# Kernel optimization log

Measured on AMD Instinct MI355X. Metric: run time of the kernel, lower is better.

The kernel has to match this reference:

```python
import jax, jax.numpy as jnp
import numpy as np

NUM_HEADS = 16
EPS = 1e-6

def _rmsnorm(h, w):
    h32 = h.astype(jnp.float32)
    var = jnp.mean(h32 * h32, axis=-1, keepdims=True)
    return (w * (h32 * jax.lax.rsqrt(var + EPS))).astype(h.dtype)

def setup_inputs() -> dict:
    key = jax.random.key(0)
    ks = jax.random.split(key, 4)
    B, N, C = 16, 1024, 1024
    x = jax.random.normal(ks[0], (B, N, C), dtype=jnp.float32)
    qkv_w = jax.random.normal(ks[1], (3 * C, C), dtype=jnp.float32) * (C ** -0.5)
    proj_w = jax.random.normal(ks[2], (C, C), dtype=jnp.float32) * (C ** -0.5)
    proj_b = jnp.zeros((C,), dtype=jnp.float32)
    q_norm_w = jnp.ones((C // NUM_HEADS,), dtype=jnp.float32)
    k_norm_w = jnp.ones((C // NUM_HEADS,), dtype=jnp.float32)
    return {"x": x, "qkv_w": qkv_w, "proj_w": proj_w, "proj_b": proj_b,
            "q_norm_w": q_norm_w, "k_norm_w": k_norm_w}

def reference(x, qkv_w, proj_w, proj_b, q_norm_w, k_norm_w):
    B, N, C = x.shape
    H = NUM_HEADS
    Dh = C // H
    scale = Dh ** -0.5  # qk_scale default; temperature = 1.0
    # QKV projection (no bias): [B,N,3,H,Dh]
    qkv = (x @ qkv_w.T).reshape(B, N, 3, H, Dh)
    q, k, v = qkv[:, :, 0], qkv[:, :, 1], qkv[:, :, 2]
    # per-head QK RMSNorm (fp32 internally)
    q = _rmsnorm(q, q_norm_w)
    k = _rmsnorm(k, k_norm_w)
    # explicit softmax attention: [B,H,N,N]
    attn = jnp.einsum('bnhd,bmhd->bhnm', q * scale, k)
    attn = jax.nn.softmax(attn, axis=-1)
    out = jnp.einsum('bhnm,bmhd->bnhd', attn, v).reshape(B, N, C)
    return out @ proj_w.T + proj_b
```

## Files before the change

kernel.cpp:

```cpp
#include <hip/hip_runtime.h>
#include <hip/hip_bf16.h>

typedef __attribute__((ext_vector_type(8))) __bf16 bf16x8;
typedef __attribute__((ext_vector_type(4))) __bf16 bf16x4;
typedef __attribute__((ext_vector_type(4))) float f32x4;

#define AS1(p) ((__attribute__((address_space(1))) void*)(p))
#define AS3(p) ((__attribute__((address_space(3))) void*)(p))

__global__ void f2b_kernel(const float4* __restrict__ in, bf16x4* __restrict__ out, int n4) {
    int idx = blockIdx.x * blockDim.x + threadIdx.x;
    int stride = gridDim.x * blockDim.x;
    for (int i = idx; i < n4; i += stride) {
        float4 v = in[i];
        bf16x4 o;
        o[0] = (__bf16)v.x; o[1] = (__bf16)v.y; o[2] = (__bf16)v.z; o[3] = (__bf16)v.w;
        out[i] = o;
    }
}

template<int MODE>
__global__ __launch_bounds__(512, 2)
void gemm256(const __bf16* __restrict__ A, const __bf16* __restrict__ Bw,
             const float* __restrict__ bias, const float* __restrict__ qw,
             const float* __restrict__ kw, float* __restrict__ Cf,
             __bf16* __restrict__ Cb, __bf16* __restrict__ Vt,
             int M, int K, int nbn, int ldc)
{
    __shared__ __bf16 Asl[4][256 * 32];
    __shared__ __bf16 Bsl[4][256 * 32];
    const int tid = threadIdx.x, l = tid & 63, w = tid >> 6;
    const int fr = l & 15, fk = l >> 4;

    const int cpx = gridDim.x >> 3;
    const int wg = (blockIdx.x & 7) * cpx + (blockIdx.x >> 3);
    const int bm = wg / nbn, bn = wg % nbn;

    const __bf16* Ag = A + (size_t)bm * 256 * K;
    const __bf16* Bg = Bw + (size_t)bn * 256 * K;

    const int arow = tid >> 2;
    const int uch = (tid & 3) ^ (arow & 3) ^ ((arow >> 2) & 3);
    const size_t ga = (size_t)arow * K + uch * 8;
    const size_t ga2 = ga + (size_t)128 * K;

    const int axc = (fk ^ (fr & 3) ^ ((fr >> 2) & 3)) * 16;
    int aoff[8], boff[4];
    #pragma unroll
    for (int m = 0; m < 8; ++m)
        aoff[m] = ((w >> 2) * 128 + m * 16 + fr) * 64 + axc;
    #pragma unroll
    for (int n = 0; n < 4; ++n)
        boff[n] = ((w & 3) * 64 + n * 16 + fr) * 64 + axc;

    f32x4 acc[8][4] = {};

#define STAGE256(S) do {                                                                    \
    const int sb_ = (S) & 3;                                                                \
    __builtin_amdgcn_global_load_lds(AS1(Ag + (size_t)(S) * 32 + ga),                       \
        AS3((char*)&Asl[sb_][0] + tid * 16), 16, 0, 0);                                     \
    __builtin_amdgcn_global_load_lds(AS1(Ag + (size_t)(S) * 32 + ga2),                      \
        AS3((char*)&Asl[sb_][0] + tid * 16 + 8192), 16, 0, 0);                              \
    __builtin_amdgcn_global_load_lds(AS1(Bg + (size_t)(S) * 32 + ga),                       \
        AS3((char*)&Bsl[sb_][0] + tid * 16), 16, 0, 0);                                     \
    __builtin_amdgcn_global_load_lds(AS1(Bg + (size_t)(S) * 32 + ga2),                      \
        AS3((char*)&Bsl[sb_][0] + tid * 16 + 8192), 16, 0, 0);                              \
} while (0)

#define PHASE256(S, VMSTR, DOSTAGE) do {                                                    \
    asm volatile("s_waitcnt vmcnt(" VMSTR ")" ::: "memory");                                \
    __builtin_amdgcn_s_barrier();                                                           \
    __builtin_amdgcn_sched_barrier(0);                                                      \
    const int pb_ = (S) & 3;                                                                \
    bf16x8 af[8], bfv[4];                                                                   \
    _Pragma("unroll")                                                                       \
    for (int m = 0; m < 8; ++m)                                                             \
        af[m] = *(const bf16x8*)((const char*)&Asl[pb_][0] + aoff[m]);                      \
    _Pragma("unroll")                                                                       \
    for (int n = 0; n < 4; ++n)                                                             \
        bfv[n] = *(const bf16x8*)((const char*)&Bsl[pb_][0] + boff[n]);                     \
    if (DOSTAGE) STAGE256((S) + 3);                                                         \
    __builtin_amdgcn_s_setprio(1);                                                          \
    _Pragma("unroll")                                                                       \
    for (int m = 0; m < 8; ++m)                                                             \
        _Pragma("unroll")                                                                   \
        for (int n = 0; n < 4; ++n)                                                         \
            acc[m][n] = __builtin_amdgcn_mfma_f32_16x16x32_bf16(af[m], bfv[n], acc[m][n], 0, 0, 0); \
    __builtin_amdgcn_s_setprio(0);                                                          \
} while (0)

    const int S = K >> 5;
    STAGE256(0); STAGE256(1); STAGE256(2);
    for (int s = 0; s < S - 2; ++s)
        PHASE256(s, "8", (s + 3 < S));
    PHASE256(S - 2, "4", false);
    PHASE256(S - 1, "0", false);
#undef PHASE256
#undef STAGE256

    const int rb0 = bm * 256 + (w >> 2) * 128 + fk * 4;
    const int cb0 = bn * 256 + (w & 3) * 64;

    if (MODE == 1) {
        #pragma unroll
        for (int m = 0; m < 8; ++m)
            #pragma unroll
            for (int n = 0; n < 4; ++n) {
                const int col = cb0 + n * 16 + fr;
                const float bv = bias[col];
                #pragma unroll
                for (int r = 0; r < 4; ++r)
                    Cf[(size_t)(rb0 + m * 16 + r) * ldc + col] = acc[m][n][r] + bv;
            }
    } else {
        const int sect = bn >> 2;
        if (sect < 2) {
            const float* wp = (sect == 0) ? qw : kw;
            float wn[4];
            #pragma unroll
            for (int n = 0; n < 4; ++n) wn[n] = wp[((w & 3) * 64 + n * 16 + fr) & 63];
            #pragma unroll
            for (int m = 0; m < 8; ++m) {
                float sc[4];
                #pragma unroll
                for (int r = 0; r < 4; ++r) {
                    float ps = 0.f;
                    #pragma unroll
                    for (int n = 0; n < 4; ++n) ps += acc[m][n][r] * acc[m][n][r];
                    ps += __shfl_xor(ps, 1); ps += __shfl_xor(ps, 2);
                    ps += __shfl_xor(ps, 4); ps += __shfl_xor(ps, 8);
                    sc[r] = rsqrtf(ps * (1.0f / 64.0f) + 1e-6f);
                    if (sect == 0) sc[r] *= 0.18033688011112042f;
                }
                #pragma unroll
                for (int n = 0; n < 4; ++n)
                    #pragma unroll
                    for (int r = 0; r < 4; ++r)
                        Cb[(size_t)(rb0 + m * 16 + r) * ldc + cb0 + n * 16 + fr] =
                            (__bf16)(acc[m][n][r] * sc[r] * wn[n]);
            }
        } else {
            #pragma unroll
            for (int m = 0; m < 8; ++m) {
                const int tok = rb0 + m * 16;
                const int b = tok >> 10, ntok = tok & 1023;
                #pragma unroll
                for (int n = 0; n < 4; ++n) {
                    const int vd = (bn - 8) * 256 + (w & 3) * 64 + n * 16 + fr;
                    bf16x4 pk;
                    #pragma unroll
                    for (int r = 0; r < 4; ++r) pk[r] = (__bf16)acc[m][n][r];
                    *(bf16x4*)&Vt[((size_t)((b * 16 + (vd >> 6)) * 64 + (vd & 63))) * 1024 + ntok] = pk;
                }
            }
        }
    }
}

__global__ __launch_bounds__(256, 3)
void attn_kernel(const __bf16* __restrict__ qkv, const __bf16* __restrict__ vt,
                 __bf16* __restrict__ ao)
{
    __shared__ __bf16 Ks[2][64 * 64];
    __shared__ __bf16 Vs[2][64 * 64];
    __shared__ __bf16 Pl[4][16 * 64];
    const int tid = threadIdx.x, l = tid & 63, w = tid >> 6;
    const int fr = l & 15, fk = l >> 4;
    const int sw = (fr & 7) << 4;

    const int bi = blockIdx.x;
    const int L = (bi & 7) * 256 + (bi >> 3);
    const int qb = L & 7, h = (L >> 3) & 15, b = L >> 7;

    const __bf16* Kg = qkv + (size_t)b * 1024 * 2048 + 1024 + h * 64;
    const __bf16* Vg = vt + (size_t)((b * 16 + h) * 64) * 1024;
    const int srow = tid >> 3, scp = tid & 7;

    const int c8 = (scp ^ (srow & 7)) * 8;
    const size_t kO0 = (size_t)srow * 2048 + c8, kO1 = kO0 + 32 * 2048;
    const size_t vO0 = (size_t)srow * 1024 + c8, vO1 = vO0 + 32 * 1024;
    char* ksd = (char*)&Ks[0][0] + tid * 16;
    char* vsd = (char*)&Vs[0][0] + tid * 16;

#define STAGE(KP, VP, BUF) do {                                                           \
    __builtin_amdgcn_global_load_lds(AS1((KP) + kO0), AS3(ksd + (BUF) * 8192), 16, 0, 0); \
    __builtin_amdgcn_global_load_lds(AS1((KP) + kO1), AS3(ksd + (BUF) * 8192 + 4096), 16, 0, 0); \
    __builtin_amdgcn_global_load_lds(AS1((VP) + vO0), AS3(vsd + (BUF) * 8192), 16, 0, 0); \
    __builtin_amdgcn_global_load_lds(AS1((VP) + vO1), AS3(vsd + (BUF) * 8192 + 4096), 16, 0, 0); \
} while (0)

    STAGE(Kg, Vg, 0);

    const int qrow0 = b * 1024 + qb * 128 + w * 32;
    bf16x8 qf[2][2];
    #pragma unroll
    for (int qi = 0; qi < 2; ++qi)
        #pragma unroll
        for (int dc = 0; dc < 2; ++dc)
            qf[qi][dc] = *(const bf16x8*)&qkv[(size_t)(qrow0 + qi * 16 + fr) * 2048
                                              + h * 64 + dc * 32 + fk * 8];

    const int kb0 = fr * 128 + ((fk ^ (fr & 7)) * 16);
    const int kb1 = fr * 128 + (((4 + fk) ^ (fr & 7)) * 16);
    const char* KsB = (const char*)&Ks[0][0];
    const char* VsB = (const char*)&Vs[0][0];

    char* Pw = (char*)&Pl[w][0];
    const int pw0 = (fr * 128 + 0 * 32 + fk * 8) ^ sw;
    const int pw1 = (fr * 128 + 1 * 32 + fk * 8) ^ sw;
    const int pw2 = (fr * 128 + 2 * 32 + fk * 8) ^ sw;
    const int pw3 = (fr * 128 + 3 * 32 + fk * 8) ^ sw;
    const int pr0 = (fr * 128 + 0 * 64 + fk * 16) ^ sw;
    const int pr1 = (fr * 128 + 1 * 64 + fk * 16) ^ sw;

    bf16x8 onesf;
    #pragma unroll
    for (int i = 0; i < 8; ++i) onesf[i] = (__bf16)1.0f;

    f32x4 oacc[2][4] = {};
    f32x4 lacc[2] = {};

    const __bf16* kg = Kg;
    const __bf16* vg = Vg;
    __syncthreads();

    for (int kt = 0; kt < 16; ++kt) {
        const int cur = kt & 1;
        if (kt < 15) { kg += 64 * 2048; vg += 64; STAGE(kg, vg, cur ^ 1); }

        const int cb = cur * 8192;
        bf16x8 kf[4][2], vf[4][2];
        #pragma unroll
        for (int n = 0; n < 4; ++n) {
            kf[n][0] = *(const bf16x8*)(KsB + cb + kb0 + n * 2048);
            kf[n][1] = *(const bf16x8*)(KsB + cb + kb1 + n * 2048);
        }
        #pragma unroll
        for (int nd = 0; nd < 4; ++nd) {
            vf[nd][0] = *(const bf16x8*)(VsB + cb + kb0 + nd * 2048);
            vf[nd][1] = *(const bf16x8*)(VsB + cb + kb1 + nd * 2048);
        }

        #pragma unroll
        for (int qi = 0; qi < 2; ++qi) {
            f32x4 sacc[4] = {};
            #pragma unroll
            for (int n = 0; n < 4; ++n)
                #pragma unroll
                for (int dc = 0; dc < 2; ++dc)
                    sacc[n] = __builtin_amdgcn_mfma_f32_16x16x32_bf16(kf[n][dc], qf[qi][dc],
                                                                      sacc[n], 0, 0, 0);

            #pragma unroll
            for (int n = 0; n < 4; ++n) {
                bf16x4 pk;
                #pragma unroll
                for (int r = 0; r < 4; ++r)
                    pk[r] = (__bf16)__builtin_amdgcn_exp2f(sacc[n][r]);
                const int pwn = (n == 0) ? pw0 : (n == 1) ? pw1 : (n == 2) ? pw2 : pw3;
                *(bf16x4*)(Pw + pwn) = pk;
            }

            bf16x8 pf0 = *(const bf16x8*)(Pw + pr0);
            bf16x8 pf1 = *(const bf16x8*)(Pw + pr1);
            lacc[qi] = __builtin_amdgcn_mfma_f32_16x16x32_bf16(pf0, onesf, lacc[qi], 0, 0, 0);
            lacc[qi] = __builtin_amdgcn_mfma_f32_16x16x32_bf16(pf1, onesf, lacc[qi], 0, 0, 0);
            #pragma unroll
            for (int nd = 0; nd < 4; ++nd) {
                oacc[qi][nd] = __builtin_amdgcn_mfma_f32_16x16x32_bf16(pf0, vf[nd][0],
                                                                       oacc[qi][nd], 0, 0, 0);
                oacc[qi][nd] = __builtin_amdgcn_mfma_f32_16x16x32_bf16(pf1, vf[nd][1],
                                                                       oacc[qi][nd], 0, 0, 0);
            }
        }
        __syncthreads();
    }

    #pragma unroll
    for (int qi = 0; qi < 2; ++qi) {
        float inv[4];
        #pragma unroll
        for (int r = 0; r < 4; ++r)
            inv[r] = __builtin_amdgcn_rcpf(lacc[qi][r]);
        #pragma unroll
        for (int nd = 0; nd < 4; ++nd)
            #pragma unroll
            for (int r = 0; r < 4; ++r)
                ao[(size_t)(qrow0 + qi * 16 + fk * 4 + r) * 1024 + h * 64 + nd * 16 + fr] =
                    (__bf16)(oacc[qi][nd][r] * inv[r]);
    }
#undef STAGE
}

extern "C" void kernel_launch(void* const* d_in, const int* in_sizes, int n_in,
                              void* d_out, int out_size, void* d_ws, size_t ws_size,
                              hipStream_t stream)
{
    const float* x      = (const float*)d_in[0];
    const float* qkv_w  = (const float*)d_in[1];
    const float* proj_w = (const float*)d_in[2];
    const float* proj_b = (const float*)d_in[3];
    const float* qnw    = (const float*)d_in[4];
    const float* knw    = (const float*)d_in[5];

    char* ws = (char*)d_ws;
    __bf16* xb    = (__bf16*)(ws);
    __bf16* wqkv  = (__bf16*)(ws + 33554432);
    __bf16* wproj = (__bf16*)(ws + 39845888);
    __bf16* qkv   = (__bf16*)(ws + 41943040);
    __bf16* vt    = (__bf16*)(ws + 109051904);
    __bf16* ao    = (__bf16*)(ws + 142606336);

    f2b_kernel<<<2048, 256, 0, stream>>>((const float4*)x,      (bf16x4*)xb,    16777216 / 4);
    f2b_kernel<<<2048, 256, 0, stream>>>((const float4*)qkv_w,  (bf16x4*)wqkv,  3145728 / 4);
    f2b_kernel<<<1024, 256, 0, stream>>>((const float4*)proj_w, (bf16x4*)wproj, 1048576 / 4);

    gemm256<0><<<768, 512, 0, stream>>>(xb, wqkv, nullptr, qnw, knw,
                                        nullptr, qkv, vt, 16384, 1024, 12, 2048);
    attn_kernel<<<2048, 256, 0, stream>>>(qkv, vt, ao);
    gemm256<1><<<256, 512, 0, stream>>>(ao, wproj, proj_b, nullptr, nullptr,
                                        (float*)d_out, nullptr, nullptr, 16384, 1024, 4, 1024);
}
```

Measured before the change: 264.8 us.

## Restructure gemm256 main loop into interleaved half-tile load/MFMA pipeline

Replaces the 4-stage K=32 ring buffer with double-buffered K=64 tiles split into two halves. Global-to-LDS loads for the next halves are interleaved between four MFMA quads per iteration, and fragment registers are halved to 4 A and 4 B vectors. The LDS swizzle pattern changes and launch bounds drop to one block per SM. The aim is better overlap of memory and MFMA work with lower register pressure, at the cost of extra barriers and possibly lower occupancy.

After: 269.5 us. About the same (+1.8%).

```diff
diff --git a/kernel.cpp b/kernel.cpp
--- a/kernel.cpp
+++ b/kernel.cpp
@@ -20,15 +20,15 @@
 }
 
 template<int MODE>
-__global__ __launch_bounds__(512, 2)
+__global__ __launch_bounds__(512, 1)
 void gemm256(const __bf16* __restrict__ A, const __bf16* __restrict__ Bw,
              const float* __restrict__ bias, const float* __restrict__ qw,
              const float* __restrict__ kw, float* __restrict__ Cf,
              __bf16* __restrict__ Cb, __bf16* __restrict__ Vt,
              int M, int K, int nbn, int ldc)
 {
-    __shared__ __bf16 Asl[4][256 * 32];
-    __shared__ __bf16 Bsl[4][256 * 32];
+    __shared__ __bf16 Asl[2][2][256 * 32];
+    __shared__ __bf16 Bsl[2][2][256 * 32];
     const int tid = threadIdx.x, l = tid & 63, w = tid >> 6;
     const int fr = l & 15, fk = l >> 4;
 
@@ -39,12 +39,12 @@
     const __bf16* Ag = A + (size_t)bm * 256 * K;
     const __bf16* Bg = Bw + (size_t)bn * 256 * K;
 
-    const int arow = tid >> 2;
-    const int uch = (tid & 3) ^ (arow & 3) ^ ((arow >> 2) & 3);
-    const size_t ga = (size_t)arow * K + uch * 8;
-    const size_t ga2 = ga + (size_t)128 * K;
-
-    const int axc = (fk ^ (fr & 3) ^ ((fr >> 2) & 3)) * 16;
+    const size_t gsb  = (size_t)(tid >> 2) * K + (((tid & 3) ^ ((tid >> 3) & 3)) * 8);
+    const size_t gsb2 = gsb + (size_t)128 * K;
+    char* const AsB = (char*)&Asl[0][0][0];
+    char* const BsB = (char*)&Bsl[0][0][0];
+
+    const int axc = (fk ^ ((fr >> 1) & 3)) * 16;
     int aoff[8], boff[4];
     #pragma unroll
     for (int m = 0; m < 8; ++m)
@@ -54,49 +54,72 @@
         boff[n] = ((w & 3) * 64 + n * 16 + fr) * 64 + axc;
 
     f32x4 acc[8][4] = {};
-
-#define STAGE256(S) do {                                                                    \
-    const int sb_ = (S) & 3;                                                                \
-    __builtin_amdgcn_global_load_lds(AS1(Ag + (size_t)(S) * 32 + ga),                       \
-        AS3((char*)&Asl[sb_][0] + tid * 16), 16, 0, 0);                                     \
-    __builtin_amdgcn_global_load_lds(AS1(Ag + (size_t)(S) * 32 + ga2),                      \
-        AS3((char*)&Asl[sb_][0] + tid * 16 + 8192), 16, 0, 0);                              \
-    __builtin_amdgcn_global_load_lds(AS1(Bg + (size_t)(S) * 32 + ga),                       \
-        AS3((char*)&Bsl[sb_][0] + tid * 16), 16, 0, 0);                                     \
-    __builtin_amdgcn_global_load_lds(AS1(Bg + (size_t)(S) * 32 + ga2),                      \
-        AS3((char*)&Bsl[sb_][0] + tid * 16 + 8192), 16, 0, 0);                              \
+    bf16x8 af[4], bf[4];
+
+#define STG(BASE, GP, KT, KH) do {                                                          \
+    char* d_ = (BASE) + (((KT) & 1) * 32768 + (KH) * 16384 + tid * 16);                     \
+    __builtin_amdgcn_global_load_lds(AS1((GP) + (size_t)(KT) * 64 + (KH) * 32 + gsb),       \
+                                     AS3(d_), 16, 0, 0);                                    \
+    __builtin_amdgcn_global_load_lds(AS1((GP) + (size_t)(KT) * 64 + (KH) * 32 + gsb2),      \
+                                     AS3(d_ + 8192), 16, 0, 0);                             \
 } while (0)
 
-#define PHASE256(S, VMSTR, DOSTAGE) do {                                                    \
-    asm volatile("s_waitcnt vmcnt(" VMSTR ")" ::: "memory");                                \
+#define MFMA_QUAD(MB) do {                                                                  \
     __builtin_amdgcn_s_barrier();                                                           \
+    asm volatile("s_waitcnt lgkmcnt(0)" ::: "memory");                                      \
     __builtin_amdgcn_sched_barrier(0);                                                      \
-    const int pb_ = (S) & 3;                                                                \
-    bf16x8 af[8], bfv[4];                                                                   \
-    _Pragma("unroll")                                                                       \
-    for (int m = 0; m < 8; ++m)                                                             \
-        af[m] = *(const bf16x8*)((const char*)&Asl[pb_][0] + aoff[m]);                      \
-    _Pragma("unroll")                                                                       \
-    for (int n = 0; n < 4; ++n)                                                             \
-        bfv[n] = *(const bf16x8*)((const char*)&Bsl[pb_][0] + boff[n]);                     \
-    if (DOSTAGE) STAGE256((S) + 3);                                                         \
     __builtin_amdgcn_s_setprio(1);                                                          \
     _Pragma("unroll")                                                                       \
-    for (int m = 0; m < 8; ++m)                                                             \
+    for (int m = 0; m < 4; ++m)                                                             \
         _Pragma("unroll")                                                                   \
         for (int n = 0; n < 4; ++n)                                                         \
-            acc[m][n] = __builtin_amdgcn_mfma_f32_16x16x32_bf16(af[m], bfv[n], acc[m][n], 0, 0, 0); \
+            acc[(MB) + m][n] = __builtin_amdgcn_mfma_f32_16x16x32_bf16(af[m], bf[n],        \
+                                                                      acc[(MB) + m][n], 0, 0, 0); \
     __builtin_amdgcn_s_setprio(0);                                                          \
+    __builtin_amdgcn_s_barrier();                                                           \
 } while (0)
 
-    const int S = K >> 5;
-    STAGE256(0); STAGE256(1); STAGE256(2);
-    for (int s = 0; s < S - 2; ++s)
-        PHASE256(s, "8", (s + 3 < S));
-    PHASE256(S - 2, "4", false);
-    PHASE256(S - 1, "0", false);
-#undef PHASE256
-#undef STAGE256
+    const int NKT = K >> 6;
+    STG(AsB, Ag, 0, 0); STG(BsB, Bg, 0, 0);
+    STG(AsB, Ag, 0, 1); STG(BsB, Bg, 0, 1);
+    STG(AsB, Ag, 1, 0); STG(BsB, Bg, 1, 0);
+    asm volatile("s_waitcnt vmcnt(4)" ::: "memory");
+    __builtin_amdgcn_s_barrier();
+
+    for (int kt = 0; kt < NKT; ++kt) {
+        const char* Ab0 = AsB + (kt & 1) * 32768;
+        const char* Bb0 = BsB + (kt & 1) * 32768;
+        #pragma unroll
+        for (int n = 0; n < 4; ++n) bf[n] = *(const bf16x8*)(Bb0 + boff[n]);
+        #pragma unroll
+        for (int m = 0; m < 4; ++m) af[m] = *(const bf16x8*)(Ab0 + aoff[m]);
+        if (kt + 1 < NKT) STG(AsB, Ag, kt + 1, 1);
+        __builtin_amdgcn_sched_barrier(0);
+        MFMA_QUAD(0);
+        #pragma unroll
+        for (int m = 0; m < 4; ++m) af[m] = *(const bf16x8*)(Ab0 + aoff[4 + m]);
+        if (kt + 1 < NKT) STG(BsB, Bg, kt + 1, 1);
+        __builtin_amdgcn_sched_barrier(0);
+        MFMA_QUAD(4);
+        const char* Ab1 = Ab0 + 16384;
+        const char* Bb1 = Bb0 + 16384;
+        #pragma unroll
+        for (int n = 0; n < 4; ++n) bf[n] = *(const bf16x8*)(Bb1 + boff[n]);
+        #pragma unroll
+        for (int m = 0; m < 4; ++m) af[m] = *(const bf16x8*)(Ab1 + aoff[m]);
+        if (kt + 2 < NKT) STG(AsB, Ag, kt + 2, 0);
+        __builtin_amdgcn_sched_barrier(0);
+        MFMA_QUAD(0);
+        #pragma unroll
+        for (int m = 0; m < 4; ++m) af[m] = *(const bf16x8*)(Ab1 + aoff[4 + m]);
+        if (kt + 2 < NKT) STG(BsB, Bg, kt + 2, 0);
+        __builtin_amdgcn_sched_barrier(0);
+        if (kt < NKT - 2) asm volatile("s_waitcnt vmcnt(4)" ::: "memory");
+        else              asm volatile("s_waitcnt vmcnt(0)" ::: "memory");
+        MFMA_QUAD(4);
+    }
+#undef MFMA_QUAD
+#undef STG
 
     const int rb0 = bm * 256 + (w >> 2) * 128 + fk * 4;
     const int cb0 = bn * 256 + (w & 3) * 64;
```
